# Optimization experiments

Hardware: AMD Instinct MI355X
Metric: run time of the kernel (lower is better)

## Reference

```python
import jax, jax.numpy as jnp
import numpy as np

B, S, H = 16, 4096, 512

def setup_inputs() -> dict:
    key = jax.random.key(0)
    k1, k2, k3, k4, k5 = jax.random.split(key, 5)
    hidden = jax.random.normal(k1, (B, H), dtype=jnp.float32)
    encoder_outputs = jax.random.normal(k2, (B, S, 2 * H), dtype=jnp.float32)
    # nn.Linear(3H, H): weight [H, 3H], bias [H]
    W_attn = jax.random.normal(k3, (H, 3 * H), dtype=jnp.float32) * (1.0 / np.sqrt(3 * H))
    b_attn = jax.random.normal(k4, (H,), dtype=jnp.float32) * 0.01
    v = jax.random.normal(k5, (H,), dtype=jnp.float32)
    return {"hidden": hidden, "encoder_outputs": encoder_outputs,
            "W_attn": W_attn, "b_attn": b_attn, "v": v}

def reference(hidden, encoder_outputs, W_attn, b_attn, v):
    src_len = encoder_outputs.shape[1]
    # [B, S, H] broadcast of decoder hidden, concat with encoder outputs -> [B, S, 3H]
    h_rep = jnp.broadcast_to(hidden[:, None, :], (hidden.shape[0], src_len, hidden.shape[1]))
    combined = jnp.concatenate([h_rep, encoder_outputs], axis=2)
    energy = jnp.tanh(jnp.einsum('bsf,hf->bsh', combined, W_attn) + b_attn)
    attention = jnp.einsum('bsh,h->bs', energy, v)  # bmm(v, energy.T) squeezed
    return jax.nn.softmax(attention, axis=1)
```

## Files before the change

### kernel.cpp

```cpp
#include <hip/hip_runtime.h>

typedef __attribute__((ext_vector_type(4))) float f32x4;
typedef __attribute__((ext_vector_type(8))) short bf16x8;

#define MEMBAR() asm volatile("" ::: "memory")

__device__ __forceinline__ unsigned short f2bf(float f) {
  unsigned int u = __builtin_bit_cast(unsigned int, f);
  u += 0x7FFFu + ((u >> 16) & 1u);
  return (unsigned short)(u >> 16);
}

__global__ __launch_bounds__(256) void k_prep_p(
    const float* __restrict__ hidden, const float* __restrict__ W,
    const float* __restrict__ bias, float* __restrict__ P) {
  __shared__ float hsh[512];
  const int b = blockIdx.x;
  for (int i = threadIdx.x; i < 512; i += 256) hsh[i] = hidden[b * 512 + i];
  __syncthreads();
  for (int h = threadIdx.x; h < 512; h += 256) {
    const float* wr = W + (long)h * 1536;
    float s = 0.f;
#pragma unroll 4
    for (int f = 0; f < 512; f += 4) {
      float4 wv = *reinterpret_cast<const float4*>(wr + f);
      s += wv.x * hsh[f] + wv.y * hsh[f + 1] + wv.z * hsh[f + 2] + wv.w * hsh[f + 3];
    }
    P[b * 512 + h] = bias[h] + s;
  }
}

__global__ __launch_bounds__(256) void k_prep_w(
    const float* __restrict__ W, unsigned short* __restrict__ W2t) {
  const int id = blockIdx.x * 256 + threadIdx.x;
  const int kk8 = (id & 3) * 8;
  const int h = (id >> 2) & 511;
  const int kb = id >> 11;
  const float* src = W + (long)h * 1536 + 512 + kb * 32 + kk8;
  float4 a = *reinterpret_cast<const float4*>(src);
  float4 c = *reinterpret_cast<const float4*>(src + 4);
  union { unsigned short u[8]; bf16x8 v; } o;
  o.u[0] = f2bf(a.x); o.u[1] = f2bf(a.y); o.u[2] = f2bf(a.z); o.u[3] = f2bf(a.w);
  o.u[4] = f2bf(c.x); o.u[5] = f2bf(c.y); o.u[6] = f2bf(c.z); o.u[7] = f2bf(c.w);
  *reinterpret_cast<bf16x8*>(W2t + (long)kb * 16384 + h * 32 + kk8) = o.v;
}

__global__ __launch_bounds__(256, 3) void k_main(
    const float* __restrict__ enc, const short* __restrict__ W2t,
    const float* __restrict__ P, const float* __restrict__ v,
    float* __restrict__ logits_part) {
  __shared__ short As[4][2048];
  __shared__ float attred[64][4];

  const int tid = threadIdx.x;
  const int lane = tid & 63;
  const int w = tid >> 6;
  const int hl = lane & 15, kg = lane >> 4;

  const int bid = blockIdx.x;
  const int xcd = bid & 7, idx = bid >> 3;
  const int mtile = xcd * 128 + (idx >> 1);
  const int ntile = idx & 1;
  const long rowbase = (long)mtile * 64;
  const int colbase = ntile * 256;
  const int b = (int)(rowbase >> 12);

  const int r = tid >> 2, c = tid & 3;
  const float* ga = enc + (rowbase + r) * 1024 + c * 8;
  const int wr_off = r * 32 + ((c ^ ((r >> 1) & 3)) << 3);
  const int base_f = hl * 32 + ((kg ^ ((hl >> 1) & 3)) << 3);
  const short* bp = W2t + (colbase + w * 64 + hl) * 32 + kg * 8;

  f32x4 acc[4][4];
#pragma unroll
  for (int mi = 0; mi < 4; ++mi)
#pragma unroll
    for (int ni = 0; ni < 4; ++ni) acc[mi][ni] = (f32x4){0.f, 0.f, 0.f, 0.f};

  bf16x8 Ba[4], Bb[4];
  f32x4 rawE0, rawE1, rawO0, rawO1;

#define CVT8W(BUF, R0, R1) {                                          \
    union { __bf16 h[8]; bf16x8 s; } _u;                              \
    _u.h[0] = (__bf16)(R0)[0]; _u.h[1] = (__bf16)(R0)[1];             \
    _u.h[2] = (__bf16)(R0)[2]; _u.h[3] = (__bf16)(R0)[3];             \
    _u.h[4] = (__bf16)(R1)[0]; _u.h[5] = (__bf16)(R1)[1];             \
    _u.h[6] = (__bf16)(R1)[2]; _u.h[7] = (__bf16)(R1)[3];             \
    *reinterpret_cast<bf16x8*>(&As[(BUF)][wr_off]) = _u.s;            \
  }
#define LOADB(DST, KB) {                                              \
    const short* _k = bp + (KB) * 16384;                              \
    DST[0] = *reinterpret_cast<const bf16x8*>(_k);                    \
    DST[1] = *reinterpret_cast<const bf16x8*>(_k + 512);              \
    DST[2] = *reinterpret_cast<const bf16x8*>(_k + 1024);             \
    DST[3] = *reinterpret_cast<const bf16x8*>(_k + 1536);             \
  }
#define MFMA16(AB, BS) {                                              \
    bf16x8 _f0 = *reinterpret_cast<const bf16x8*>((AB) + base_f);     \
    bf16x8 _f1 = *reinterpret_cast<const bf16x8*>((AB) + base_f + 512); \
    bf16x8 _f2 = *reinterpret_cast<const bf16x8*>((AB) + base_f + 1024); \
    bf16x8 _f3 = *reinterpret_cast<const bf16x8*>((AB) + base_f + 1536); \
    acc[0][0] = __builtin_amdgcn_mfma_f32_16x16x32_bf16(_f0, BS[0], acc[0][0], 0, 0, 0); \
    acc[0][1] = __builtin_amdgcn_mfma_f32_16x16x32_bf16(_f0, BS[1], acc[0][1], 0, 0, 0); \
    acc[0][2] = __builtin_amdgcn_mfma_f32_16x16x32_bf16(_f0, BS[2], acc[0][2], 0, 0, 0); \
    acc[0][3] = __builtin_amdgcn_mfma_f32_16x16x32_bf16(_f0, BS[3], acc[0][3], 0, 0, 0); \
    acc[1][0] = __builtin_amdgcn_mfma_f32_16x16x32_bf16(_f1, BS[0], acc[1][0], 0, 0, 0); \
    acc[1][1] = __builtin_amdgcn_mfma_f32_16x16x32_bf16(_f1, BS[1], acc[1][1], 0, 0, 0); \
    acc[1][2] = __builtin_amdgcn_mfma_f32_16x16x32_bf16(_f1, BS[2], acc[1][2], 0, 0, 0); \
    acc[1][3] = __builtin_amdgcn_mfma_f32_16x16x32_bf16(_f1, BS[3], acc[1][3], 0, 0, 0); \
    acc[2][0] = __builtin_amdgcn_mfma_f32_16x16x32_bf16(_f2, BS[0], acc[2][0], 0, 0, 0); \
    acc[2][1] = __builtin_amdgcn_mfma_f32_16x16x32_bf16(_f2, BS[1], acc[2][1], 0, 0, 0); \
    acc[2][2] = __builtin_amdgcn_mfma_f32_16x16x32_bf16(_f2, BS[2], acc[2][2], 0, 0, 0); \
    acc[2][3] = __builtin_amdgcn_mfma_f32_16x16x32_bf16(_f2, BS[3], acc[2][3], 0, 0, 0); \
    acc[3][0] = __builtin_amdgcn_mfma_f32_16x16x32_bf16(_f3, BS[0], acc[3][0], 0, 0, 0); \
    acc[3][1] = __builtin_amdgcn_mfma_f32_16x16x32_bf16(_f3, BS[1], acc[3][1], 0, 0, 0); \
    acc[3][2] = __builtin_amdgcn_mfma_f32_16x16x32_bf16(_f3, BS[2], acc[3][2], 0, 0, 0); \
    acc[3][3] = __builtin_amdgcn_mfma_f32_16x16x32_bf16(_f3, BS[3], acc[3][3], 0, 0, 0); \
  }
#define K_ITER(J, RC0, RC1, RL0, RL1, BIN, BOUT, DO_G, DO_B, DO_CVT) {\
    MEMBAR();                                                         \
    __builtin_amdgcn_s_barrier();                                     \
    MEMBAR();                                                         \
    if (DO_G) {                                                       \
      RL0 = *reinterpret_cast<const f32x4*>(ga + ((J) + 2) * 32);     \
      RL1 = *reinterpret_cast<const f32x4*>(ga + ((J) + 2) * 32 + 4); \
    }                                                                 \
    if (DO_B) LOADB(BOUT, (J) + 1);                                   \
    MEMBAR();                                                         \
    MFMA16(&As[(J) & 3][0], BIN)                                      \
    if (DO_CVT) CVT8W(((J) + 1) & 3, RC0, RC1);                       \
    asm volatile("s_waitcnt lgkmcnt(0)" ::: "memory");                \
  }

  rawE0 = *reinterpret_cast<const f32x4*>(ga);
  rawE1 = *reinterpret_cast<const f32x4*>(ga + 4);
  CVT8W(0, rawE0, rawE1);
  rawO0 = *reinterpret_cast<const f32x4*>(ga + 32);
  rawO1 = *reinterpret_cast<const f32x4*>(ga + 36);
  LOADB(Ba, 0);
  __syncthreads();

#pragma unroll 1
  for (int p = 0; p < 15; ++p) {
    const int j = p * 2;
    K_ITER(j,     rawO0, rawO1, rawE0, rawE1, Ba, Bb, 1, 1, 1)
    K_ITER(j + 1, rawE0, rawE1, rawO0, rawO1, Bb, Ba, 1, 1, 1)
  }
  K_ITER(30, rawO0, rawO1, rawE0, rawE1, Ba, Bb, 0, 1, 1)
  K_ITER(31, rawE0, rawE1, rawO0, rawO1, Bb, Ba, 0, 0, 0)

#undef K_ITER
#undef MFMA16
#undef LOADB
#undef CVT8W

  float part[4][4];
#pragma unroll
  for (int mi = 0; mi < 4; ++mi)
#pragma unroll
    for (int rr = 0; rr < 4; ++rr) part[mi][rr] = 0.f;

#pragma unroll
  for (int ni = 0; ni < 4; ++ni) {
    const int h = colbase + w * 64 + ni * 16 + hl;
    const float ph = P[b * 512 + h];
    const float vh = v[h];
#pragma unroll
    for (int mi = 0; mi < 4; ++mi)
#pragma unroll
      for (int rr = 0; rr < 4; ++rr) {
        float x = acc[mi][ni][rr] + ph;
        float e = __expf(2.f * x);
        part[mi][rr] += vh * (1.f - 2.f * __frcp_rn(e + 1.f));
      }
  }
#pragma unroll
  for (int off = 1; off < 16; off <<= 1)
#pragma unroll
    for (int mi = 0; mi < 4; ++mi)
#pragma unroll
      for (int rr = 0; rr < 4; ++rr)
        part[mi][rr] += __shfl_xor(part[mi][rr], off, 16);

  __syncthreads();
  if (hl == 0) {
#pragma unroll
    for (int mi = 0; mi < 4; ++mi)
#pragma unroll
      for (int rr = 0; rr < 4; ++rr)
        attred[mi * 16 + kg * 4 + rr][w] = part[mi][rr];
  }
  __syncthreads();
  if (tid < 64) {
    const float* a = attred[tid];
    logits_part[ntile * 65536 + rowbase + tid] =
        (a[0] + a[1]) + (a[2] + a[3]);
  }
}

__global__ __launch_bounds__(256) void k_softmax(
    const float* __restrict__ logits_part, float* __restrict__ out) {
  const int b = blockIdx.x;
  const int t = threadIdx.x;
  const int wid = t >> 6, lane = t & 63;
  const float* L0 = logits_part + b * 4096;
  const float* L1 = logits_part + 65536 + b * 4096;
  __shared__ float rmax[4], rsum[4];
  float lv[16];
  float m = -1e30f;
#pragma unroll
  for (int i = 0; i < 16; ++i) {
    const int j = t + i * 256;
    lv[i] = L0[j] + L1[j];
    m = fmaxf(m, lv[i]);
  }
#pragma unroll
  for (int off = 32; off >= 1; off >>= 1) m = fmaxf(m, __shfl_xor(m, off));
  if (lane == 0) rmax[wid] = m;
  __syncthreads();
  m = fmaxf(fmaxf(rmax[0], rmax[1]), fmaxf(rmax[2], rmax[3]));
  float s = 0.f;
#pragma unroll
  for (int i = 0; i < 16; ++i) {
    lv[i] = __expf(lv[i] - m);
    s += lv[i];
  }
#pragma unroll
  for (int off = 32; off >= 1; off >>= 1) s += __shfl_xor(s, off);
  if (lane == 0) rsum[wid] = s;
  __syncthreads();
  s = rsum[0] + rsum[1] + rsum[2] + rsum[3];
  float inv = 1.0f / s;
#pragma unroll
  for (int i = 0; i < 16; ++i) out[b * 4096 + t + i * 256] = lv[i] * inv;
}

extern "C" void kernel_launch(void* const* d_in, const int* in_sizes, int n_in,
                              void* d_out, int out_size, void* d_ws, size_t ws_size,
                              hipStream_t stream) {
  const float* hidden = (const float*)d_in[0];
  const float* enc    = (const float*)d_in[1];
  const float* W      = (const float*)d_in[2];
  const float* bias   = (const float*)d_in[3];
  const float* v      = (const float*)d_in[4];
  float* out = (float*)d_out;

  char* ws = (char*)d_ws;
  float* P = (float*)ws;
  unsigned short* W2t = (unsigned short*)(ws + 32768);
  float* logits_part = (float*)(ws + 32768 + 1048576);

  k_prep_p<<<16, 256, 0, stream>>>(hidden, W, bias, P);
  k_prep_w<<<256, 256, 0, stream>>>(W, W2t);
  k_main<<<2048, 256, 0, stream>>>(enc, (const short*)W2t, P, v, logits_part);
  k_softmax<<<16, 256, 0, stream>>>(logits_part, out);
}
```

Baseline: 146.9 us.

## Deepen k_main software pipeline with register-prefetched LDS fragments and triple-buffered globals

The main GEMM loop is restructured so A fragments are prefetched from LDS into registers one iteration ahead (Fa/Fb ping-pong). B tiles are now loaded two k-steps ahead, and three raw encoder f32 chunks are kept in flight, five steps ahead, instead of two. The aim is to hide LDS and global-memory latency behind the MFMA chain. It raises register use considerably, so the launch bound occupancy hint drops from 3 to 2 blocks per CU, which trades occupancy for deeper per-wave pipelining.

```diff
diff --git a/kernel.cpp b/kernel.cpp
--- a/kernel.cpp
+++ b/kernel.cpp
@@ -45,7 +45,7 @@
   *reinterpret_cast<bf16x8*>(W2t + (long)kb * 16384 + h * 32 + kk8) = o.v;
 }
 
-__global__ __launch_bounds__(256, 3) void k_main(
+__global__ __launch_bounds__(256, 2) void k_main(
     const float* __restrict__ enc, const short* __restrict__ W2t,
     const float* __restrict__ P, const float* __restrict__ v,
     float* __restrict__ logits_part) {
@@ -78,7 +78,8 @@
     for (int ni = 0; ni < 4; ++ni) acc[mi][ni] = (f32x4){0.f, 0.f, 0.f, 0.f};
 
   bf16x8 Ba[4], Bb[4];
-  f32x4 rawE0, rawE1, rawO0, rawO1;
+  bf16x8 Fa[4], Fb[4];
+  f32x4 raw0a, raw0b, raw1a, raw1b, raw2a, raw2b;
 
 #define CVT8W(BUF, R0, R1) {                                          \
     union { __bf16 h[8]; bf16x8 s; } _u;                              \
@@ -95,61 +96,93 @@
     DST[2] = *reinterpret_cast<const bf16x8*>(_k + 1024);             \
     DST[3] = *reinterpret_cast<const bf16x8*>(_k + 1536);             \
   }
-#define MFMA16(AB, BS) {                                              \
-    bf16x8 _f0 = *reinterpret_cast<const bf16x8*>((AB) + base_f);     \
-    bf16x8 _f1 = *reinterpret_cast<const bf16x8*>((AB) + base_f + 512); \
-    bf16x8 _f2 = *reinterpret_cast<const bf16x8*>((AB) + base_f + 1024); \
-    bf16x8 _f3 = *reinterpret_cast<const bf16x8*>((AB) + base_f + 1536); \
-    acc[0][0] = __builtin_amdgcn_mfma_f32_16x16x32_bf16(_f0, BS[0], acc[0][0], 0, 0, 0); \
-    acc[0][1] = __builtin_amdgcn_mfma_f32_16x16x32_bf16(_f0, BS[1], acc[0][1], 0, 0, 0); \
-    acc[0][2] = __builtin_amdgcn_mfma_f32_16x16x32_bf16(_f0, BS[2], acc[0][2], 0, 0, 0); \
-    acc[0][3] = __builtin_amdgcn_mfma_f32_16x16x32_bf16(_f0, BS[3], acc[0][3], 0, 0, 0); \
-    acc[1][0] = __builtin_amdgcn_mfma_f32_16x16x32_bf16(_f1, BS[0], acc[1][0], 0, 0, 0); \
-    acc[1][1] = __builtin_amdgcn_mfma_f32_16x16x32_bf16(_f1, BS[1], acc[1][1], 0, 0, 0); \
-    acc[1][2] = __builtin_amdgcn_mfma_f32_16x16x32_bf16(_f1, BS[2], acc[1][2], 0, 0, 0); \
-    acc[1][3] = __builtin_amdgcn_mfma_f32_16x16x32_bf16(_f1, BS[3], acc[1][3], 0, 0, 0); \
-    acc[2][0] = __builtin_amdgcn_mfma_f32_16x16x32_bf16(_f2, BS[0], acc[2][0], 0, 0, 0); \
-    acc[2][1] = __builtin_amdgcn_mfma_f32_16x16x32_bf16(_f2, BS[1], acc[2][1], 0, 0, 0); \
-    acc[2][2] = __builtin_amdgcn_mfma_f32_16x16x32_bf16(_f2, BS[2], acc[2][2], 0, 0, 0); \
-    acc[2][3] = __builtin_amdgcn_mfma_f32_16x16x32_bf16(_f2, BS[3], acc[2][3], 0, 0, 0); \
-    acc[3][0] = __builtin_amdgcn_mfma_f32_16x16x32_bf16(_f3, BS[0], acc[3][0], 0, 0, 0); \
-    acc[3][1] = __builtin_amdgcn_mfma_f32_16x16x32_bf16(_f3, BS[1], acc[3][1], 0, 0, 0); \
-    acc[3][2] = __builtin_amdgcn_mfma_f32_16x16x32_bf16(_f3, BS[2], acc[3][2], 0, 0, 0); \
-    acc[3][3] = __builtin_amdgcn_mfma_f32_16x16x32_bf16(_f3, BS[3], acc[3][3], 0, 0, 0); \
-  }
-#define K_ITER(J, RC0, RC1, RL0, RL1, BIN, BOUT, DO_G, DO_B, DO_CVT) {\
+#define MFMA16(FS, BS) {                                              \
+    acc[0][0] = __builtin_amdgcn_mfma_f32_16x16x32_bf16(FS[0], BS[0], acc[0][0], 0, 0, 0); \
+    acc[0][1] = __builtin_amdgcn_mfma_f32_16x16x32_bf16(FS[0], BS[1], acc[0][1], 0, 0, 0); \
+    acc[0][2] = __builtin_amdgcn_mfma_f32_16x16x32_bf16(FS[0], BS[2], acc[0][2], 0, 0, 0); \
+    acc[0][3] = __builtin_amdgcn_mfma_f32_16x16x32_bf16(FS[0], BS[3], acc[0][3], 0, 0, 0); \
+    acc[1][0] = __builtin_amdgcn_mfma_f32_16x16x32_bf16(FS[1], BS[0], acc[1][0], 0, 0, 0); \
+    acc[1][1] = __builtin_amdgcn_mfma_f32_16x16x32_bf16(FS[1], BS[1], acc[1][1], 0, 0, 0); \
+    acc[1][2] = __builtin_amdgcn_mfma_f32_16x16x32_bf16(FS[1], BS[2], acc[1][2], 0, 0, 0); \
+    acc[1][3] = __builtin_amdgcn_mfma_f32_16x16x32_bf16(FS[1], BS[3], acc[1][3], 0, 0, 0); \
+    acc[2][0] = __builtin_amdgcn_mfma_f32_16x16x32_bf16(FS[2], BS[0], acc[2][0], 0, 0, 0); \
+    acc[2][1] = __builtin_amdgcn_mfma_f32_16x16x32_bf16(FS[2], BS[1], acc[2][1], 0, 0, 0); \
+    acc[2][2] = __builtin_amdgcn_mfma_f32_16x16x32_bf16(FS[2], BS[2], acc[2][2], 0, 0, 0); \
+    acc[2][3] = __builtin_amdgcn_mfma_f32_16x16x32_bf16(FS[2], BS[3], acc[2][3], 0, 0, 0); \
+    acc[3][0] = __builtin_amdgcn_mfma_f32_16x16x32_bf16(FS[3], BS[0], acc[3][0], 0, 0, 0); \
+    acc[3][1] = __builtin_amdgcn_mfma_f32_16x16x32_bf16(FS[3], BS[1], acc[3][1], 0, 0, 0); \
+    acc[3][2] = __builtin_amdgcn_mfma_f32_16x16x32_bf16(FS[3], BS[2], acc[3][2], 0, 0, 0); \
+    acc[3][3] = __builtin_amdgcn_mfma_f32_16x16x32_bf16(FS[3], BS[3], acc[3][3], 0, 0, 0); \
+  }
+#define K_IT(J, RC0, RC1, FIN, FOUT, BIO, DO_G, DO_B, DO_CVT, DO_F) { \
     MEMBAR();                                                         \
     __builtin_amdgcn_s_barrier();                                     \
     MEMBAR();                                                         \
+    if (DO_F) {                                                       \
+      const short* _fb = &As[((J) + 1) & 3][0];                       \
+      FOUT[0] = *reinterpret_cast<const bf16x8*>(_fb + base_f);       \
+      FOUT[1] = *reinterpret_cast<const bf16x8*>(_fb + base_f + 512); \
+      FOUT[2] = *reinterpret_cast<const bf16x8*>(_fb + base_f + 1024);\
+      FOUT[3] = *reinterpret_cast<const bf16x8*>(_fb + base_f + 1536);\
+    }                                                                 \
+    MFMA16(FIN, BIO)                                                  \
+    if (DO_CVT) CVT8W(((J) + 2) & 3, RC0, RC1);                       \
     if (DO_G) {                                                       \
-      RL0 = *reinterpret_cast<const f32x4*>(ga + ((J) + 2) * 32);     \
-      RL1 = *reinterpret_cast<const f32x4*>(ga + ((J) + 2) * 32 + 4); \
+      RC0 = *reinterpret_cast<const f32x4*>(ga + ((J) + 5) * 32);     \
+      RC1 = *reinterpret_cast<const f32x4*>(ga + ((J) + 5) * 32 + 4); \
     }                                                                 \
-    if (DO_B) LOADB(BOUT, (J) + 1);                                   \
-    MEMBAR();                                                         \
-    MFMA16(&As[(J) & 3][0], BIN)                                      \
-    if (DO_CVT) CVT8W(((J) + 1) & 3, RC0, RC1);                       \
+    if (DO_B) LOADB(BIO, (J) + 2);                                    \
     asm volatile("s_waitcnt lgkmcnt(0)" ::: "memory");                \
   }
 
-  rawE0 = *reinterpret_cast<const f32x4*>(ga);
-  rawE1 = *reinterpret_cast<const f32x4*>(ga + 4);
-  CVT8W(0, rawE0, rawE1);
-  rawO0 = *reinterpret_cast<const f32x4*>(ga + 32);
-  rawO1 = *reinterpret_cast<const f32x4*>(ga + 36);
+  {
+    f32x4 t0 = *reinterpret_cast<const f32x4*>(ga);
+    f32x4 t1 = *reinterpret_cast<const f32x4*>(ga + 4);
+    CVT8W(0, t0, t1);
+    f32x4 t2 = *reinterpret_cast<const f32x4*>(ga + 32);
+    f32x4 t3 = *reinterpret_cast<const f32x4*>(ga + 36);
+    CVT8W(1, t2, t3);
+  }
+  raw0a = *reinterpret_cast<const f32x4*>(ga + 64);
+  raw0b = *reinterpret_cast<const f32x4*>(ga + 68);
+  raw1a = *reinterpret_cast<const f32x4*>(ga + 96);
+  raw1b = *reinterpret_cast<const f32x4*>(ga + 100);
+  raw2a = *reinterpret_cast<const f32x4*>(ga + 128);
+  raw2b = *reinterpret_cast<const f32x4*>(ga + 132);
   LOADB(Ba, 0);
-  __syncthreads();
+  LOADB(Bb, 1);
+  __syncthreads();
+  Fa[0] = *reinterpret_cast<const bf16x8*>(&As[0][0] + base_f);
+  Fa[1] = *reinterpret_cast<const bf16x8*>(&As[0][0] + base_f + 512);
+  Fa[2] = *reinterpret_cast<const bf16x8*>(&As[0][0] + base_f + 1024);
+  Fa[3] = *reinterpret_cast<const bf16x8*>(&As[0][0] + base_f + 1536);
 
 #pragma unroll 1
-  for (int p = 0; p < 15; ++p) {
-    const int j = p * 2;
-    K_ITER(j,     rawO0, rawO1, rawE0, rawE1, Ba, Bb, 1, 1, 1)
-    K_ITER(j + 1, rawE0, rawE1, rawO0, rawO1, Bb, Ba, 1, 1, 1)
-  }
-  K_ITER(30, rawO0, rawO1, rawE0, rawE1, Ba, Bb, 0, 1, 1)
-  K_ITER(31, rawE0, rawE1, rawO0, rawO1, Bb, Ba, 0, 0, 0)
-
-#undef K_ITER
+  for (int p = 0; p < 2; ++p) {
+    const int j = p * 12;
+    K_IT(j + 0,  raw0a, raw0b, Fa, Fb, Ba, 1, 1, 1, 1)
+    K_IT(j + 1,  raw1a, raw1b, Fb, Fa, Bb, 1, 1, 1, 1)
+    K_IT(j + 2,  raw2a, raw2b, Fa, Fb, Ba, 1, 1, 1, 1)
+    K_IT(j + 3,  raw0a, raw0b, Fb, Fa, Bb, 1, 1, 1, 1)
+    K_IT(j + 4,  raw1a, raw1b, Fa, Fb, Ba, 1, 1, 1, 1)
+    K_IT(j + 5,  raw2a, raw2b, Fb, Fa, Bb, 1, 1, 1, 1)
+    K_IT(j + 6,  raw0a, raw0b, Fa, Fb, Ba, 1, 1, 1, 1)
+    K_IT(j + 7,  raw1a, raw1b, Fb, Fa, Bb, 1, 1, 1, 1)
+    K_IT(j + 8,  raw2a, raw2b, Fa, Fb, Ba, 1, 1, 1, 1)
+    K_IT(j + 9,  raw0a, raw0b, Fb, Fa, Bb, 1, 1, 1, 1)
+    K_IT(j + 10, raw1a, raw1b, Fa, Fb, Ba, 1, 1, 1, 1)
+    K_IT(j + 11, raw2a, raw2b, Fb, Fa, Bb, 1, 1, 1, 1)
+  }
+  K_IT(24, raw0a, raw0b, Fa, Fb, Ba, 1, 1, 1, 1)
+  K_IT(25, raw1a, raw1b, Fb, Fa, Bb, 1, 1, 1, 1)
+  K_IT(26, raw2a, raw2b, Fa, Fb, Ba, 1, 1, 1, 1)
+  K_IT(27, raw0a, raw0b, Fb, Fa, Bb, 0, 1, 1, 1)
+  K_IT(28, raw1a, raw1b, Fa, Fb, Ba, 0, 1, 1, 1)
+  K_IT(29, raw2a, raw2b, Fb, Fa, Bb, 0, 1, 1, 1)
+  K_IT(30, raw0a, raw0b, Fa, Fb, Ba, 0, 0, 0, 1)
+  K_IT(31, raw0a, raw0b, Fb, Fa, Bb, 0, 0, 0, 0)
+
+#undef K_IT
 #undef MFMA16
 #undef LOADB
 #undef CVT8W
```

New measurement: 153.0 us. 1.04x slower.
